# Kernel optimization log

Hardware: AMD Instinct MI355X
Metric: run time of the kernel (lower is better)

Reference implementation:

```python
import jax, jax.numpy as jnp
import numpy as np

N_HEAD, D_MODEL, D_HEAD, D_INNER = 16, 1024, 64, 4096
QLEN, BSZ = 2048, 2
LN_EPS = 1e-5
NEG_MIN = np.float32(np.finfo(np.float32).min)


def layer_norm(x, g, b, eps=LN_EPS):
    mu = jnp.mean(x, axis=-1, keepdims=True)
    var = jnp.var(x, axis=-1, keepdims=True)
    return (x - mu) * jax.lax.rsqrt(var + eps) * g + b


def rel_shift_uni(x):
    # x: [q, k, b, n] -> Transformer-XL relative shift
    q, k, b, n = x.shape
    zero_pad = jnp.zeros((q, 1, b, n), dtype=x.dtype)
    x_padded = jnp.concatenate([zero_pad, x], axis=1)        # [q, k+1, b, n]
    x_padded = x_padded.reshape(k + 1, q, b, n)
    return x_padded[1:].reshape(q, k, b, n)


def setup_inputs() -> dict:
    key = jax.random.key(0)
    ks = jax.random.split(key, 16)
    s = 0.02
    inp = {
        "dec_inp": jax.random.normal(ks[0], (QLEN, BSZ, D_MODEL), jnp.float32),
        "r": jax.random.normal(ks[1], (QLEN, D_MODEL), jnp.float32),
        "r_w_bias": jax.random.normal(ks[2], (N_HEAD, D_HEAD), jnp.float32) * s,
        "r_r_bias": jax.random.normal(ks[3], (N_HEAD, D_HEAD), jnp.float32) * s,
        "qkv_w": jax.random.normal(ks[4], (3 * N_HEAD * D_HEAD, D_MODEL), jnp.float32) * s,
        "r_net_w": jax.random.normal(ks[5], (N_HEAD * D_HEAD, D_MODEL), jnp.float32) * s,
        "o_w": jax.random.normal(ks[6], (D_MODEL, N_HEAD * D_HEAD), jnp.float32) * s,
        "ln_attn_g": jnp.ones((D_MODEL,), jnp.float32),
        "ln_attn_b": jnp.zeros((D_MODEL,), jnp.float32),
        "w1": jax.random.normal(ks[7], (D_INNER, D_MODEL), jnp.float32) * s,
        "b1": jnp.zeros((D_INNER,), jnp.float32),
        "w2": jax.random.normal(ks[8], (D_MODEL, D_INNER), jnp.float32) * s,
        "b2": jnp.zeros((D_MODEL,), jnp.float32),
        "ln_ff_g": jnp.ones((D_MODEL,), jnp.float32),
        "ln_ff_b": jnp.zeros((D_MODEL,), jnp.float32),
        # causal mask: mask position j > i; shape [q, k, 1]
        "attn_mask": jnp.triu(jnp.ones((QLEN, QLEN), bool), k=1)[:, :, None],
    }
    return inp


def reference(dec_inp, r, r_w_bias, r_r_bias, qkv_w, r_net_w, o_w,
              ln_attn_g, ln_attn_b, w1, b1, w2, b2, ln_ff_g, ln_ff_b,
              attn_mask):
    qlen, bsz = dec_inp.shape[0], dec_inp.shape[1]
    scale = 1.0 / (D_HEAD ** 0.5)

    # QKV projection (post-LN: no pre-norm)
    w_heads = jnp.einsum('ibm,hm->ibh', dec_inp, qkv_w)  # [q, b, 3*n*d]
    w_head_q, w_head_k, w_head_v = jnp.split(w_heads, 3, axis=-1)
    w_head_q = w_head_q.reshape(qlen, bsz, N_HEAD, D_HEAD)
    w_head_k = w_head_k.reshape(qlen, bsz, N_HEAD, D_HEAD)
    w_head_v = w_head_v.reshape(qlen, bsz, N_HEAD, D_HEAD)

    # content attention score (AC)
    rw_head_q = w_head_q + r_w_bias                      # [q, b, n, d]
    attn_score = jnp.einsum('ibnd,jbnd->ijbn', rw_head_q, w_head_k)

    # position attention score (BD) with relative shift
    rr_head_q = w_head_q + r_r_bias
    r_head_k = jnp.einsum('jm,hm->jh', r, r_net_w).reshape(qlen, N_HEAD, D_HEAD)
    BD = jnp.einsum('ibnd,jnd->ijbn', rr_head_q, r_head_k)
    BD = rel_shift_uni(BD)

    attn_score = (attn_score + BD) * scale
    attn_score = jnp.where(attn_mask[:, :, :, None], NEG_MIN, attn_score)

    attn_prob = jax.nn.softmax(attn_score, axis=1)       # softmax over key dim
    attn_vec = jnp.einsum('ijbn,jbnd->ibnd', attn_prob, w_head_v)
    attn_vec = attn_vec.reshape(qlen, bsz, N_HEAD * D_HEAD)
    attn_out = jnp.einsum('ibh,mh->ibm', attn_vec, o_w)

    # post-LN residual
    output = layer_norm(dec_inp + attn_out, ln_attn_g, ln_attn_b)

    # Positionwise FFN (post-LN)
    hidden = jax.nn.relu(jnp.einsum('ibm,fm->ibf', output, w1) + b1)
    core_out = jnp.einsum('ibf,mf->ibm', hidden, w2) + b2
    output = layer_norm(output + core_out, ln_ff_g, ln_ff_b)
    return output
```

## Files before the change

### kernel.cpp

```cpp
#include <hip/hip_runtime.h>
#include <stdint.h>

#define QL 2048
#define NHEAD 16
#define DHEAD 64
#define DMODEL 1024
#define DINNER 4096

typedef __attribute__((ext_vector_type(8))) short bf16x8;
typedef __attribute__((ext_vector_type(4))) float f32x4;

__device__ __forceinline__ ushort f2bf(float f) {
  uint32_t u = __float_as_uint(f);
  u = (u + 0x7fffu + ((u >> 16) & 1u)) >> 16;
  return (ushort)u;
}
__device__ __forceinline__ float bf2f(ushort u) {
  return __uint_as_float(((uint32_t)u) << 16);
}

__device__ __forceinline__ void gload_lds16(const void* g, void* l) {
  auto gp = reinterpret_cast<const uint32_t __attribute__((address_space(1)))*>(
      reinterpret_cast<uintptr_t>(g));
  auto lp = reinterpret_cast<uint32_t __attribute__((address_space(3)))*>(
      (uint32_t)reinterpret_cast<uintptr_t>(l));
  __builtin_amdgcn_global_load_lds(gp, lp, 16, 0, 0);
}

__global__ __launch_bounds__(256) void cvt_bf16_k(const float* __restrict__ in,
                                                  ushort* __restrict__ out, int n4) {
  int i = blockIdx.x * 256 + threadIdx.x;
  if (i < n4) {
    float4 v = ((const float4*)in)[i];
    ushort4 u;
    u.x = f2bf(v.x); u.y = f2bf(v.y); u.z = f2bf(v.z); u.w = f2bf(v.w);
    ((ushort4*)out)[i] = u;
  }
}

#define EPI_QKV 0
#define EPI_RK 1
#define EPI_F32 2
#define EPI_RELU_BF16 3
#define EPI_BIAS_F32 4

template <int EPI>
__global__ __launch_bounds__(256) void gemm_nt(
    const ushort* __restrict__ A, const ushort* __restrict__ B, int M, int N, int K,
    float* __restrict__ Cf, ushort* __restrict__ Cb, const float* __restrict__ bias,
    ushort* __restrict__ qw, ushort* __restrict__ qr, ushort* __restrict__ kbuf,
    ushort* __restrict__ vt, const float* __restrict__ rwb, const float* __restrict__ rrb) {
  __shared__ ushort As[2][128 * 32];
  __shared__ ushort Bs[2][128 * 32];
  const int t = threadIdx.x;
  const int lane = t & 63, wv = t >> 6;
  const int wr = wv >> 1, wc = wv & 1;
  const int m0 = blockIdx.y * 128, n0 = blockIdx.x * 128;
  const int rif = lane & 15;
  const int kb = (lane >> 4) * 16;

  f32x4 acc[4][4] = {};
  const char* Ab = (const char*)A;
  const char* Bb = (const char*)B;
  const int arow = t >> 2;
  const int acol = (t & 3) * 16;

  auto stage = [&](int b, int k0) {
    size_t abase = ((size_t)(m0 + arow) * K + k0) * 2 + acol;
    gload_lds16(Ab + abase, (char*)As[b] + t * 16);
    gload_lds16(Ab + abase + (size_t)64 * K * 2, (char*)As[b] + t * 16 + 4096);
    size_t bbase = ((size_t)(n0 + arow) * K + k0) * 2 + acol;
    gload_lds16(Bb + bbase, (char*)Bs[b] + t * 16);
    gload_lds16(Bb + bbase + (size_t)64 * K * 2, (char*)Bs[b] + t * 16 + 4096);
  };

  stage(0, 0);
  asm volatile("s_waitcnt vmcnt(0)" ::: "memory");
  __builtin_amdgcn_s_barrier();
  __builtin_amdgcn_sched_barrier(0);

  int cur = 0;
#pragma unroll 1
  for (int k0 = 0; k0 < K; k0 += 32) {
    if (k0 + 32 < K) stage(cur ^ 1, k0 + 32);
    bf16x8 af[4], bfr[4];
#pragma unroll
    for (int m = 0; m < 4; m++)
      af[m] = *(const bf16x8*)((const char*)As[cur] + (wr * 64 + m * 16 + rif) * 64 + kb);
#pragma unroll
    for (int n = 0; n < 4; n++)
      bfr[n] = *(const bf16x8*)((const char*)Bs[cur] + (wc * 64 + n * 16 + rif) * 64 + kb);
    __builtin_amdgcn_s_setprio(1);
#pragma unroll
    for (int m = 0; m < 4; m++)
#pragma unroll
      for (int n = 0; n < 4; n++)
        acc[m][n] = __builtin_amdgcn_mfma_f32_16x16x32_bf16(af[m], bfr[n], acc[m][n], 0, 0, 0);
    __builtin_amdgcn_s_setprio(0);
    asm volatile("s_waitcnt vmcnt(0)" ::: "memory");
    __builtin_amdgcn_s_barrier();
    __builtin_amdgcn_sched_barrier(0);
    cur ^= 1;
  }

  const int rbase = (lane >> 4) * 4;
#pragma unroll
  for (int m = 0; m < 4; m++) {
#pragma unroll
    for (int n = 0; n < 4; n++) {
#pragma unroll
      for (int reg = 0; reg < 4; reg++) {
        int gr = m0 + wr * 64 + m * 16 + rbase + reg;
        int gc = n0 + wc * 64 + n * 16 + (lane & 15);
        float v = acc[m][n][reg];
        if (EPI == EPI_F32) {
          Cf[(size_t)gr * N + gc] = v;
        } else if (EPI == EPI_BIAS_F32) {
          Cf[(size_t)gr * N + gc] = v + bias[gc];
        } else if (EPI == EPI_RELU_BF16) {
          Cb[(size_t)gr * N + gc] = f2bf(fmaxf(v + bias[gc], 0.f));
        } else if (EPI == EPI_RK) {
          int hn = gc >> 6, hd = gc & 63;
          Cb[((size_t)hn * QL + gr) * 64 + hd] = f2bf(v);
        } else {
          int which = gc >> 10, hh = gc & 1023;
          int hn = hh >> 6, hd = hh & 63;
          int qi = gr >> 1, qb = gr & 1;
          size_t off = ((size_t)(qb * NHEAD + hn) * QL + qi) * 64 + hd;
          if (which == 0) {
            qw[off] = f2bf(v + rwb[hh]);
            qr[off] = f2bf(v + rrb[hh]);
          } else if (which == 1) {
            kbuf[off] = f2bf(v);
          } else {
            vt[((size_t)(qb * NHEAD + hn) * 64 + hd) * QL + qi] = f2bf(v);
          }
        }
      }
    }
  }
}

template <int EPI>
__global__ __launch_bounds__(256) void gemm_nt64(
    const ushort* __restrict__ A, const ushort* __restrict__ B, int M, int N, int K,
    float* __restrict__ Cf, ushort* __restrict__ Cb, const float* __restrict__ bias) {
  __shared__ ushort As[2][128 * 32];
  __shared__ ushort Bs[2][64 * 32];
  const int t = threadIdx.x;
  const int lane = t & 63, wv = t >> 6;
  const int wr = wv >> 1, wc = wv & 1;
  const int m0 = blockIdx.y * 128, n0 = blockIdx.x * 64;
  const int rif = lane & 15;
  const int kb = (lane >> 4) * 16;

  f32x4 acc[4][2] = {};
  const char* Ab = (const char*)A;
  const char* Bb = (const char*)B;
  const int arow = t >> 2;
  const int acol = (t & 3) * 16;

  auto stage = [&](int b, int k0) {
    size_t abase = ((size_t)(m0 + arow) * K + k0) * 2 + acol;
    gload_lds16(Ab + abase, (char*)As[b] + t * 16);
    gload_lds16(Ab + abase + (size_t)64 * K * 2, (char*)As[b] + t * 16 + 4096);
    size_t bbase = ((size_t)(n0 + arow) * K + k0) * 2 + acol;
    gload_lds16(Bb + bbase, (char*)Bs[b] + t * 16);
  };

  stage(0, 0);
  asm volatile("s_waitcnt vmcnt(0)" ::: "memory");
  __builtin_amdgcn_s_barrier();
  __builtin_amdgcn_sched_barrier(0);

  int cur = 0;
#pragma unroll 1
  for (int k0 = 0; k0 < K; k0 += 32) {
    if (k0 + 32 < K) stage(cur ^ 1, k0 + 32);
    bf16x8 af[4], bfr[2];
#pragma unroll
    for (int m = 0; m < 4; m++)
      af[m] = *(const bf16x8*)((const char*)As[cur] + (wr * 64 + m * 16 + rif) * 64 + kb);
#pragma unroll
    for (int n = 0; n < 2; n++)
      bfr[n] = *(const bf16x8*)((const char*)Bs[cur] + (wc * 32 + n * 16 + rif) * 64 + kb);
    __builtin_amdgcn_s_setprio(1);
#pragma unroll
    for (int m = 0; m < 4; m++)
#pragma unroll
      for (int n = 0; n < 2; n++)
        acc[m][n] = __builtin_amdgcn_mfma_f32_16x16x32_bf16(af[m], bfr[n], acc[m][n], 0, 0, 0);
    __builtin_amdgcn_s_setprio(0);
    asm volatile("s_waitcnt vmcnt(0)" ::: "memory");
    __builtin_amdgcn_s_barrier();
    __builtin_amdgcn_sched_barrier(0);
    cur ^= 1;
  }

  const int rbase = (lane >> 4) * 4;
#pragma unroll
  for (int m = 0; m < 4; m++) {
#pragma unroll
    for (int n = 0; n < 2; n++) {
#pragma unroll
      for (int reg = 0; reg < 4; reg++) {
        int gr = m0 + wr * 64 + m * 16 + rbase + reg;
        int gc = n0 + wc * 32 + n * 16 + (lane & 15);
        float v = acc[m][n][reg];
        if (EPI == EPI_F32) {
          Cf[(size_t)gr * N + gc] = v;
        } else if (EPI == EPI_BIAS_F32) {
          Cf[(size_t)gr * N + gc] = v + bias[gc];
        } else {
          int hn = gc >> 6, hd = gc & 63;
          Cb[((size_t)hn * QL + gr) * 64 + hd] = f2bf(v);
        }
      }
    }
  }
}

__global__ __launch_bounds__(256) void flash_attn(
    const ushort* __restrict__ Qw, const ushort* __restrict__ Qr,
    const ushort* __restrict__ Kb, const ushort* __restrict__ Vt,
    const ushort* __restrict__ Rk, ushort* __restrict__ out) {
  __shared__ ushort K_lds[2][64 * 64];
  __shared__ ushort V_lds[2][64 * 64];
  __shared__ ushort R_lds[2][128 * 64];
  __shared__ ushort P_lds[4][16 * 64];

  const int t = threadIdx.x;
  const int lane = t & 63, wv = t >> 6;
  const int bn = blockIdx.y;
  const int qb = bn >> 4, hn = bn & 15;
  const int c4 = lane & 15, g4 = lane >> 4;

  const char* Qwb = (const char*)(Qw + (size_t)bn * QL * 64);
  const char* Qrb = (const char*)(Qr + (size_t)bn * QL * 64);
  const char* Kbb = (const char*)(Kb + (size_t)bn * QL * 64);
  const char* Vtb = (const char*)(Vt + (size_t)bn * 64 * QL);
  const char* Rkb = (const char*)(Rk + (size_t)hn * QL * 64);

  int addrs[4];
#pragma unroll
  for (int reg = 0; reg < 4; reg++) {
    int rr = g4 * 4 + reg;
    addrs[reg] = ((lane & 48) | ((c4 + 15 - rr) & 15)) << 2;
  }

  const float SCALE2 = 0.125f * 1.44269504088896340736f;

#pragma unroll 1
  for (int ph = 0; ph < 2; ph++) {
    const int itile = (ph == 0) ? (31 - (int)blockIdx.x) : (int)blockIdx.x;
    const int i0 = itile * 64;
    const int iw = i0 + wv * 16;
    const int niter = itile + 1;

    bf16x8 qwf[2], qrf[2];
#pragma unroll
    for (int kk = 0; kk < 2; kk++) {
      qwf[kk] = *(const bf16x8*)(Qwb + (size_t)(iw + c4) * 128 + kk * 64 + g4 * 16);
      qrf[kk] = *(const bf16x8*)(Qrb + (size_t)(iw + c4) * 128 + kk * 64 + g4 * 16);
    }

    f32x4 o_acc[4] = {};
    float m_run[4], l_run[4];
#pragma unroll
    for (int r = 0; r < 4; r++) { m_run[r] = -3.0e38f; l_run[r] = 0.f; }

    auto stage = [&](int b, int j0) {
      const int T0 = j0 - i0 + (QL - 64);
#pragma unroll
      for (int p = 0; p < 2; p++) {
        int o = t * 16 + p * 4096;
        int row = o >> 7, ch16 = ((((o & 127) >> 4) ^ (row & 7)) << 4);
        gload_lds16(Kbb + (size_t)(j0 + row) * 128 + ch16, (char*)K_lds[b] + o);
        gload_lds16(Vtb + (size_t)row * (QL * 2) + (size_t)j0 * 2 + ch16, (char*)V_lds[b] + o);
      }
#pragma unroll
      for (int p = 0; p < 4; p++) {
        int o = t * 16 + p * 4096;
        int r = o >> 7;
        int srow = T0 + r; srow = srow > QL - 1 ? QL - 1 : srow;
        int ch16 = ((((o & 127) >> 4) ^ (r & 7)) << 4);
        gload_lds16(Rkb + (size_t)srow * 128 + ch16, (char*)R_lds[b] + o);
      }
    };

    stage(0, 0);
    asm volatile("s_waitcnt vmcnt(0)" ::: "memory");
    __builtin_amdgcn_s_barrier();
    __builtin_amdgcn_sched_barrier(0);

    int cur = 0;
#pragma unroll 1
    for (int it = 0; it < niter; ++it) {
      const int j0 = it * 64;
      if (it + 1 < niter) stage(cur ^ 1, j0 + 64);

      f32x4 acc_s[4] = {};
      f32x4 acc_bd[5] = {};
      const int baseloc = 48 - wv * 16;
      __builtin_amdgcn_s_setprio(1);
#pragma unroll
      for (int kk = 0; kk < 2; kk++) {
        const int sw = (((kk * 4 + g4) ^ (c4 & 7)) << 4);
#pragma unroll
        for (int nf = 0; nf < 4; nf++) {
          bf16x8 bk = *(const bf16x8*)((const char*)K_lds[cur] + (nf * 16 + c4) * 128 + sw);
          acc_s[nf] = __builtin_amdgcn_mfma_f32_16x16x32_bf16(qwf[kk], bk, acc_s[nf], 0, 0, 0);
        }
#pragma unroll
        for (int tf = 0; tf < 5; tf++) {
          int oo = baseloc + tf * 16 + c4;
          bf16x8 br = *(const bf16x8*)((const char*)R_lds[cur] + oo * 128 + sw);
          acc_bd[tf] = __builtin_amdgcn_mfma_f32_16x16x32_bf16(qrf[kk], br, acc_bd[tf], 0, 0, 0);
        }
      }
      __builtin_amdgcn_s_setprio(0);

      uint32_t pk[4][4];
#pragma unroll
      for (int nf = 0; nf < 4; nf++)
#pragma unroll
        for (int reg = 0; reg < 4; reg++)
          asm("v_cvt_pk_bf16_f32 %0, %1, %2"
              : "=v"(pk[nf][reg])
              : "v"(acc_bd[nf][reg]), "v"(acc_bd[nf + 1][reg]));

      float sv[4][4];
      float rowmax[4] = {-3.0e38f, -3.0e38f, -3.0e38f, -3.0e38f};
#pragma unroll
      for (int nf = 0; nf < 4; nf++) {
#pragma unroll
        for (int reg = 0; reg < 4; reg++) {
          int rr = g4 * 4 + reg;
          int jg = j0 + nf * 16 + c4;
          int ig = iw + rr;
          uint32_t pulled = (uint32_t)__builtin_amdgcn_ds_bpermute(addrs[reg], (int)pk[nf][reg]);
          uint32_t bits = (c4 > rr) ? (pulled & 0xffff0000u) : (pulled << 16);
          float v = (acc_s[nf][reg] + __uint_as_float(bits)) * SCALE2;
          v = (jg <= ig) ? v : -3.0e38f;
          sv[nf][reg] = v;
          rowmax[reg] = fmaxf(rowmax[reg], v);
        }
      }
#pragma unroll
      for (int reg = 0; reg < 4; reg++) {
        float rm = rowmax[reg];
        rm = fmaxf(rm, __shfl_xor(rm, 1));
        rm = fmaxf(rm, __shfl_xor(rm, 2));
        rm = fmaxf(rm, __shfl_xor(rm, 4));
        rm = fmaxf(rm, __shfl_xor(rm, 8));
        float mnew = fmaxf(m_run[reg], rm);
        float alpha = __builtin_amdgcn_exp2f(m_run[reg] - mnew);
        float rsum = 0.f;
#pragma unroll
        for (int nf = 0; nf < 4; nf++) {
          float p = __builtin_amdgcn_exp2f(sv[nf][reg] - mnew);
          sv[nf][reg] = p;
          rsum += p;
        }
        rsum += __shfl_xor(rsum, 1);
        rsum += __shfl_xor(rsum, 2);
        rsum += __shfl_xor(rsum, 4);
        rsum += __shfl_xor(rsum, 8);
        l_run[reg] = l_run[reg] * alpha + rsum;
        m_run[reg] = mnew;
#pragma unroll
        for (int df = 0; df < 4; df++) o_acc[df][reg] *= alpha;
      }

      {
        char* pb = (char*)P_lds[wv];
#pragma unroll
        for (int nf = 0; nf < 4; nf++)
#pragma unroll
          for (int reg = 0; reg < 4; reg++) {
            int row = g4 * 4 + reg, col = nf * 16 + c4;
            int byt = row * 128 + ((((col >> 3) ^ (row & 7))) << 4) + (col & 7) * 2;
            *(ushort*)(pb + byt) = f2bf(sv[nf][reg]);
          }
      }
      __builtin_amdgcn_s_setprio(1);
#pragma unroll
      for (int kk = 0; kk < 2; kk++) {
        const char* pb = (const char*)P_lds[wv];
        bf16x8 pa = *(const bf16x8*)(pb + c4 * 128 + (((kk * 4 + g4) ^ (c4 & 7)) << 4));
        const int sw = (((kk * 4 + g4) ^ (c4 & 7)) << 4);
#pragma unroll
        for (int df = 0; df < 4; df++) {
          bf16x8 bv = *(const bf16x8*)((const char*)V_lds[cur] + (df * 16 + c4) * 128 + sw);
          o_acc[df] = __builtin_amdgcn_mfma_f32_16x16x32_bf16(pa, bv, o_acc[df], 0, 0, 0);
        }
      }
      __builtin_amdgcn_s_setprio(0);

      asm volatile("s_waitcnt vmcnt(0)" ::: "memory");
      __builtin_amdgcn_s_barrier();
      __builtin_amdgcn_sched_barrier(0);
      cur ^= 1;
    }

#pragma unroll
    for (int reg = 0; reg < 4; reg++) {
      float inv = 1.0f / l_run[reg];
      int ig = iw + g4 * 4 + reg;
      size_t grow = (size_t)(ig * 2 + qb) * 1024 + hn * 64;
#pragma unroll
      for (int df = 0; df < 4; df++)
        out[grow + df * 16 + c4] = f2bf(o_acc[df][reg] * inv);
    }
  }
}

template <bool WB>
__global__ __launch_bounds__(256) void ln_res(
    const float* __restrict__ xa, const float* __restrict__ xb,
    const float* __restrict__ g, const float* __restrict__ bt,
    float* __restrict__ of, ushort* __restrict__ ob) {
  __shared__ float red[8];
  const int row = blockIdx.x;
  const int t = threadIdx.x;
  const int lane = t & 63, wv = t >> 6;
  const float4 a = *(const float4*)(xa + (size_t)row * 1024 + t * 4);
  const float4 c = *(const float4*)(xb + (size_t)row * 1024 + t * 4);
  float x[4] = {a.x + c.x, a.y + c.y, a.z + c.z, a.w + c.w};
  float s = x[0] + x[1] + x[2] + x[3];
  for (int m = 1; m < 64; m <<= 1) s += __shfl_xor(s, m);
  if (lane == 0) red[wv] = s;
  __syncthreads();
  float mu = (red[0] + red[1] + red[2] + red[3]) * (1.f / 1024.f);
  float d[4];
  float ss = 0.f;
#pragma unroll
  for (int i = 0; i < 4; i++) { d[i] = x[i] - mu; ss += d[i] * d[i]; }
  for (int m = 1; m < 64; m <<= 1) ss += __shfl_xor(ss, m);
  if (lane == 0) red[4 + wv] = ss;
  __syncthreads();
  float var = (red[4] + red[5] + red[6] + red[7]) * (1.f / 1024.f);
  float rs = rsqrtf(var + 1e-5f);
  float4 gv = *(const float4*)(g + t * 4);
  float4 bv = *(const float4*)(bt + t * 4);
  float y[4] = {d[0] * rs * gv.x + bv.x, d[1] * rs * gv.y + bv.y,
                d[2] * rs * gv.z + bv.z, d[3] * rs * gv.w + bv.w};
  float4 yo = make_float4(y[0], y[1], y[2], y[3]);
  *(float4*)(of + (size_t)row * 1024 + t * 4) = yo;
  if (WB) {
    ushort4 u;
    u.x = f2bf(y[0]); u.y = f2bf(y[1]); u.z = f2bf(y[2]); u.w = f2bf(y[3]);
    *(ushort4*)(ob + (size_t)row * 1024 + t * 4) = u;
  }
}

extern "C" void kernel_launch(void* const* d_in, const int* in_sizes, int n_in,
                              void* d_out, int out_size, void* d_ws, size_t ws_size,
                              hipStream_t stream) {
  const float* dec_inp = (const float*)d_in[0];
  const float* r_in = (const float*)d_in[1];
  const float* rwb = (const float*)d_in[2];
  const float* rrb = (const float*)d_in[3];
  const float* qkv_w = (const float*)d_in[4];
  const float* rnet_w = (const float*)d_in[5];
  const float* o_w = (const float*)d_in[6];
  const float* ln_attn_g = (const float*)d_in[7];
  const float* ln_attn_b = (const float*)d_in[8];
  const float* w1 = (const float*)d_in[9];
  const float* b1 = (const float*)d_in[10];
  const float* w2 = (const float*)d_in[11];
  const float* b2 = (const float*)d_in[12];
  const float* ln_ff_g = (const float*)d_in[13];
  const float* ln_ff_b = (const float*)d_in[14];
  float* out = (float*)d_out;

  char* ws = (char*)d_ws;
  size_t off = 0;
  auto alloc = [&](size_t bytes) {
    char* p = ws + off;
    off += (bytes + 255) & ~(size_t)255;
    return p;
  };
  const int ROWS = QL * 2;
  ushort* qkvw_b = (ushort*)alloc((size_t)3072 * 1024 * 2);
  ushort* rnetw_b = (ushort*)alloc((size_t)1024 * 1024 * 2);
  ushort* ow_b = (ushort*)alloc((size_t)1024 * 1024 * 2);
  ushort* w1_b = (ushort*)alloc((size_t)4096 * 1024 * 2);
  ushort* w2_b = (ushort*)alloc((size_t)1024 * 4096 * 2);
  ushort* x_b = (ushort*)alloc((size_t)ROWS * 1024 * 2);
  ushort* r_b = (ushort*)alloc((size_t)QL * 1024 * 2);
  ushort* Qw = (ushort*)alloc((size_t)32 * QL * 64 * 2);
  ushort* Qr = (ushort*)alloc((size_t)32 * QL * 64 * 2);
  ushort* Kb = (ushort*)alloc((size_t)32 * QL * 64 * 2);
  ushort* Vt = (ushort*)alloc((size_t)32 * 64 * QL * 2);
  ushort* rk = (ushort*)alloc((size_t)16 * QL * 64 * 2);
  ushort* avec = (ushort*)alloc((size_t)ROWS * 1024 * 2);
  float* attn_out = (float*)alloc((size_t)ROWS * 1024 * 4);
  float* x1f = (float*)alloc((size_t)ROWS * 1024 * 4);
  ushort* x1b = (ushort*)alloc((size_t)ROWS * 1024 * 2);
  ushort* hidden = (ushort*)alloc((size_t)ROWS * 4096 * 2);
  float* core = (float*)alloc((size_t)ROWS * 1024 * 4);

  auto cvt = [&](const float* src, ushort* dst, int n) {
    int n4 = n / 4;
    cvt_bf16_k<<<n4 / 256, 256, 0, stream>>>(src, dst, n4);
  };
  cvt(qkv_w, qkvw_b, 3072 * 1024);
  cvt(rnet_w, rnetw_b, 1024 * 1024);
  cvt(o_w, ow_b, 1024 * 1024);
  cvt(w1, w1_b, 4096 * 1024);
  cvt(w2, w2_b, 1024 * 4096);
  cvt(dec_inp, x_b, ROWS * 1024);
  cvt(r_in, r_b, QL * 1024);

  gemm_nt<EPI_QKV><<<dim3(3072 / 128, ROWS / 128), 256, 0, stream>>>(
      x_b, qkvw_b, ROWS, 3072, 1024, nullptr, nullptr, nullptr, Qw, Qr, Kb, Vt, rwb, rrb);
  gemm_nt64<EPI_RK><<<dim3(1024 / 64, QL / 128), 256, 0, stream>>>(
      r_b, rnetw_b, QL, 1024, 1024, nullptr, rk, nullptr);
  flash_attn<<<dim3(16, 32), 256, 0, stream>>>(Qw, Qr, Kb, Vt, rk, avec);
  gemm_nt64<EPI_F32><<<dim3(1024 / 64, ROWS / 128), 256, 0, stream>>>(
      avec, ow_b, ROWS, 1024, 1024, attn_out, nullptr, nullptr);
  ln_res<true><<<ROWS, 256, 0, stream>>>(dec_inp, attn_out, ln_attn_g, ln_attn_b, x1f, x1b);
  gemm_nt<EPI_RELU_BF16><<<dim3(4096 / 128, ROWS / 128), 256, 0, stream>>>(
      x1b, w1_b, ROWS, 4096, 1024, nullptr, hidden, b1, nullptr, nullptr, nullptr, nullptr,
      nullptr, nullptr);
  gemm_nt64<EPI_BIAS_F32><<<dim3(1024 / 64, ROWS / 128), 256, 0, stream>>>(
      hidden, w2_b, ROWS, 1024, 4096, core, nullptr, b2);
  ln_res<false><<<ROWS, 256, 0, stream>>>(x1f, core, ln_ff_g, ln_ff_b, out, nullptr);
}
```

Measured before the change: 358.4 us.

## Split-K output GEMMs, smaller-tile r-projection, and single fused conversion kernel

Measured after the change: 350.1 us. 2.3% less time.

```diff
diff --git a/kernel.cpp b/kernel.cpp
--- a/kernel.cpp
+++ b/kernel.cpp
@@ -14,9 +14,6 @@
   uint32_t u = __float_as_uint(f);
   u = (u + 0x7fffu + ((u >> 16) & 1u)) >> 16;
   return (ushort)u;
-}
-__device__ __forceinline__ float bf2f(ushort u) {
-  return __uint_as_float(((uint32_t)u) << 16);
 }
 
 __device__ __forceinline__ void gload_lds16(const void* g, void* l) {
@@ -27,22 +24,29 @@
   __builtin_amdgcn_global_load_lds(gp, lp, 16, 0, 0);
 }
 
-__global__ __launch_bounds__(256) void cvt_bf16_k(const float* __restrict__ in,
-                                                  ushort* __restrict__ out, int n4) {
-  int i = blockIdx.x * 256 + threadIdx.x;
-  if (i < n4) {
-    float4 v = ((const float4*)in)[i];
+struct CvtArgs {
+  const float* src[7];
+  ushort* dst[7];
+  int end[7];
+};
+
+__global__ __launch_bounds__(256) void cvt_all_k(CvtArgs a, int total4) {
+  for (int i = blockIdx.x * 256 + threadIdx.x; i < total4; i += gridDim.x * 256) {
+    int seg = 0;
+#pragma unroll
+    for (int s = 0; s < 6; s++)
+      if (i >= a.end[s]) seg = s + 1;
+    int base = seg ? a.end[seg - 1] : 0;
+    int j = i - base;
+    float4 v = ((const float4*)a.src[seg])[j];
     ushort4 u;
     u.x = f2bf(v.x); u.y = f2bf(v.y); u.z = f2bf(v.z); u.w = f2bf(v.w);
-    ((ushort4*)out)[i] = u;
+    ((ushort4*)a.dst[seg])[j] = u;
   }
 }
 
 #define EPI_QKV 0
-#define EPI_RK 1
-#define EPI_F32 2
 #define EPI_RELU_BF16 3
-#define EPI_BIAS_F32 4
 
 template <int EPI>
 __global__ __launch_bounds__(256) void gemm_nt(
@@ -113,15 +117,8 @@
         int gr = m0 + wr * 64 + m * 16 + rbase + reg;
         int gc = n0 + wc * 64 + n * 16 + (lane & 15);
         float v = acc[m][n][reg];
-        if (EPI == EPI_F32) {
-          Cf[(size_t)gr * N + gc] = v;
-        } else if (EPI == EPI_BIAS_F32) {
-          Cf[(size_t)gr * N + gc] = v + bias[gc];
-        } else if (EPI == EPI_RELU_BF16) {
+        if (EPI == EPI_RELU_BF16) {
           Cb[(size_t)gr * N + gc] = f2bf(fmaxf(v + bias[gc], 0.f));
-        } else if (EPI == EPI_RK) {
-          int hn = gc >> 6, hd = gc & 63;
-          Cb[((size_t)hn * QL + gr) * 64 + hd] = f2bf(v);
         } else {
           int which = gc >> 10, hh = gc & 1023;
           int hn = hh >> 6, hd = hh & 63;
@@ -141,16 +138,20 @@
   }
 }
 
-template <int EPI>
-__global__ __launch_bounds__(256) void gemm_nt64(
-    const ushort* __restrict__ A, const ushort* __restrict__ B, int M, int N, int K,
-    float* __restrict__ Cf, ushort* __restrict__ Cb, const float* __restrict__ bias) {
+template <int WITH_BIAS>
+__global__ __launch_bounds__(256) void gemm_nt64sk(
+    const ushort* __restrict__ A, const ushort* __restrict__ B, int M, int N, int Kfull,
+    int Klen, float* __restrict__ Cf0, float* __restrict__ Cf1,
+    const float* __restrict__ bias) {
   __shared__ ushort As[2][128 * 32];
   __shared__ ushort Bs[2][64 * 32];
   const int t = threadIdx.x;
   const int lane = t & 63, wv = t >> 6;
   const int wr = wv >> 1, wc = wv & 1;
   const int m0 = blockIdx.y * 128, n0 = blockIdx.x * 64;
+  const int z = blockIdx.z;
+  const int koff = z * Klen;
+  float* Cf = z ? Cf1 : Cf0;
   const int rif = lane & 15;
   const int kb = (lane >> 4) * 16;
 
@@ -161,10 +162,10 @@
   const int acol = (t & 3) * 16;
 
   auto stage = [&](int b, int k0) {
-    size_t abase = ((size_t)(m0 + arow) * K + k0) * 2 + acol;
+    size_t abase = ((size_t)(m0 + arow) * Kfull + koff + k0) * 2 + acol;
     gload_lds16(Ab + abase, (char*)As[b] + t * 16);
-    gload_lds16(Ab + abase + (size_t)64 * K * 2, (char*)As[b] + t * 16 + 4096);
-    size_t bbase = ((size_t)(n0 + arow) * K + k0) * 2 + acol;
+    gload_lds16(Ab + abase + (size_t)64 * Kfull * 2, (char*)As[b] + t * 16 + 4096);
+    size_t bbase = ((size_t)(n0 + arow) * Kfull + koff + k0) * 2 + acol;
     gload_lds16(Bb + bbase, (char*)Bs[b] + t * 16);
   };
 
@@ -175,8 +176,8 @@
 
   int cur = 0;
 #pragma unroll 1
-  for (int k0 = 0; k0 < K; k0 += 32) {
-    if (k0 + 32 < K) stage(cur ^ 1, k0 + 32);
+  for (int k0 = 0; k0 < Klen; k0 += 32) {
+    if (k0 + 32 < Klen) stage(cur ^ 1, k0 + 32);
     bf16x8 af[4], bfr[2];
 #pragma unroll
     for (int m = 0; m < 4; m++)
@@ -207,14 +208,78 @@
         int gr = m0 + wr * 64 + m * 16 + rbase + reg;
         int gc = n0 + wc * 32 + n * 16 + (lane & 15);
         float v = acc[m][n][reg];
-        if (EPI == EPI_F32) {
-          Cf[(size_t)gr * N + gc] = v;
-        } else if (EPI == EPI_BIAS_F32) {
-          Cf[(size_t)gr * N + gc] = v + bias[gc];
-        } else {
-          int hn = gc >> 6, hd = gc & 63;
-          Cb[((size_t)hn * QL + gr) * 64 + hd] = f2bf(v);
-        }
+        if (WITH_BIAS && z == 0) v += bias[gc];
+        Cf[(size_t)gr * N + gc] = v;
+      }
+    }
+  }
+}
+
+__global__ __launch_bounds__(256) void gemm_rk64(
+    const ushort* __restrict__ A, const ushort* __restrict__ B, int M, int N, int K,
+    ushort* __restrict__ Cb) {
+  __shared__ ushort As[2][64 * 32];
+  __shared__ ushort Bs[2][64 * 32];
+  const int t = threadIdx.x;
+  const int lane = t & 63, wv = t >> 6;
+  const int wr = wv >> 1, wc = wv & 1;
+  const int m0 = blockIdx.y * 64, n0 = blockIdx.x * 64;
+  const int rif = lane & 15;
+  const int kb = (lane >> 4) * 16;
+
+  f32x4 acc[2][2] = {};
+  const char* Ab = (const char*)A;
+  const char* Bb = (const char*)B;
+  const int arow = t >> 2;
+  const int acol = (t & 3) * 16;
+
+  auto stage = [&](int b, int k0) {
+    size_t abase = ((size_t)(m0 + arow) * K + k0) * 2 + acol;
+    gload_lds16(Ab + abase, (char*)As[b] + t * 16);
+    size_t bbase = ((size_t)(n0 + arow) * K + k0) * 2 + acol;
+    gload_lds16(Bb + bbase, (char*)Bs[b] + t * 16);
+  };
+
+  stage(0, 0);
+  asm volatile("s_waitcnt vmcnt(0)" ::: "memory");
+  __builtin_amdgcn_s_barrier();
+  __builtin_amdgcn_sched_barrier(0);
+
+  int cur = 0;
+#pragma unroll 1
+  for (int k0 = 0; k0 < K; k0 += 32) {
+    if (k0 + 32 < K) stage(cur ^ 1, k0 + 32);
+    bf16x8 af[2], bfr[2];
+#pragma unroll
+    for (int m = 0; m < 2; m++)
+      af[m] = *(const bf16x8*)((const char*)As[cur] + (wr * 32 + m * 16 + rif) * 64 + kb);
+#pragma unroll
+    for (int n = 0; n < 2; n++)
+      bfr[n] = *(const bf16x8*)((const char*)Bs[cur] + (wc * 32 + n * 16 + rif) * 64 + kb);
+    __builtin_amdgcn_s_setprio(1);
+#pragma unroll
+    for (int m = 0; m < 2; m++)
+#pragma unroll
+      for (int n = 0; n < 2; n++)
+        acc[m][n] = __builtin_amdgcn_mfma_f32_16x16x32_bf16(af[m], bfr[n], acc[m][n], 0, 0, 0);
+    __builtin_amdgcn_s_setprio(0);
+    asm volatile("s_waitcnt vmcnt(0)" ::: "memory");
+    __builtin_amdgcn_s_barrier();
+    __builtin_amdgcn_sched_barrier(0);
+    cur ^= 1;
+  }
+
+  const int rbase = (lane >> 4) * 4;
+#pragma unroll
+  for (int m = 0; m < 2; m++) {
+#pragma unroll
+    for (int n = 0; n < 2; n++) {
+#pragma unroll
+      for (int reg = 0; reg < 4; reg++) {
+        int gr = m0 + wr * 32 + m * 16 + rbase + reg;
+        int gc = n0 + wc * 32 + n * 16 + (lane & 15);
+        int hn = gc >> 6, hd = gc & 63;
+        Cb[((size_t)hn * QL + gr) * 64 + hd] = f2bf(acc[m][n][reg]);
       }
     }
   }
@@ -416,17 +481,18 @@
 }
 
 template <bool WB>
-__global__ __launch_bounds__(256) void ln_res(
-    const float* __restrict__ xa, const float* __restrict__ xb,
-    const float* __restrict__ g, const float* __restrict__ bt,
-    float* __restrict__ of, ushort* __restrict__ ob) {
+__global__ __launch_bounds__(256) void ln_res3(
+    const float* __restrict__ xa, const float* __restrict__ xb0,
+    const float* __restrict__ xb1, const float* __restrict__ g,
+    const float* __restrict__ bt, float* __restrict__ of, ushort* __restrict__ ob) {
   __shared__ float red[8];
   const int row = blockIdx.x;
   const int t = threadIdx.x;
   const int lane = t & 63, wv = t >> 6;
   const float4 a = *(const float4*)(xa + (size_t)row * 1024 + t * 4);
-  const float4 c = *(const float4*)(xb + (size_t)row * 1024 + t * 4);
-  float x[4] = {a.x + c.x, a.y + c.y, a.z + c.z, a.w + c.w};
+  const float4 c0 = *(const float4*)(xb0 + (size_t)row * 1024 + t * 4);
+  const float4 c1 = *(const float4*)(xb1 + (size_t)row * 1024 + t * 4);
+  float x[4] = {a.x + c0.x + c1.x, a.y + c0.y + c1.y, a.z + c0.z + c1.z, a.w + c0.w + c1.w};
   float s = x[0] + x[1] + x[2] + x[3];
   for (int m = 1; m < 64; m <<= 1) s += __shfl_xor(s, m);
   if (lane == 0) red[wv] = s;
@@ -495,36 +561,39 @@
   ushort* Vt = (ushort*)alloc((size_t)32 * 64 * QL * 2);
   ushort* rk = (ushort*)alloc((size_t)16 * QL * 64 * 2);
   ushort* avec = (ushort*)alloc((size_t)ROWS * 1024 * 2);
-  float* attn_out = (float*)alloc((size_t)ROWS * 1024 * 4);
+  float* p0 = (float*)alloc((size_t)ROWS * 1024 * 4);
+  float* p1 = (float*)alloc((size_t)ROWS * 1024 * 4);
   float* x1f = (float*)alloc((size_t)ROWS * 1024 * 4);
   ushort* x1b = (ushort*)alloc((size_t)ROWS * 1024 * 2);
   ushort* hidden = (ushort*)alloc((size_t)ROWS * 4096 * 2);
-  float* core = (float*)alloc((size_t)ROWS * 1024 * 4);
-
-  auto cvt = [&](const float* src, ushort* dst, int n) {
-    int n4 = n / 4;
-    cvt_bf16_k<<<n4 / 256, 256, 0, stream>>>(src, dst, n4);
-  };
-  cvt(qkv_w, qkvw_b, 3072 * 1024);
-  cvt(rnet_w, rnetw_b, 1024 * 1024);
-  cvt(o_w, ow_b, 1024 * 1024);
-  cvt(w1, w1_b, 4096 * 1024);
-  cvt(w2, w2_b, 1024 * 4096);
-  cvt(dec_inp, x_b, ROWS * 1024);
-  cvt(r_in, r_b, QL * 1024);
+  float* q0 = (float*)alloc((size_t)ROWS * 1024 * 4);
+  float* q1 = (float*)alloc((size_t)ROWS * 1024 * 4);
+
+  CvtArgs ca;
+  int n4[7] = {3072 * 1024 / 4, 1024 * 1024 / 4, 1024 * 1024 / 4, 4096 * 1024 / 4,
+               1024 * 4096 / 4, ROWS * 1024 / 4, QL * 1024 / 4};
+  const float* srcs[7] = {qkv_w, rnet_w, o_w, w1, w2, dec_inp, r_in};
+  ushort* dsts[7] = {qkvw_b, rnetw_b, ow_b, w1_b, w2_b, x_b, r_b};
+  int cum = 0;
+  for (int i = 0; i < 7; i++) {
+    ca.src[i] = srcs[i];
+    ca.dst[i] = dsts[i];
+    cum += n4[i];
+    ca.end[i] = cum;
+  }
+  cvt_all_k<<<2048, 256, 0, stream>>>(ca, cum);
 
   gemm_nt<EPI_QKV><<<dim3(3072 / 128, ROWS / 128), 256, 0, stream>>>(
       x_b, qkvw_b, ROWS, 3072, 1024, nullptr, nullptr, nullptr, Qw, Qr, Kb, Vt, rwb, rrb);
-  gemm_nt64<EPI_RK><<<dim3(1024 / 64, QL / 128), 256, 0, stream>>>(
-      r_b, rnetw_b, QL, 1024, 1024, nullptr, rk, nullptr);
+  gemm_rk64<<<dim3(1024 / 64, QL / 64), 256, 0, stream>>>(r_b, rnetw_b, QL, 1024, 1024, rk);
   flash_attn<<<dim3(16, 32), 256, 0, stream>>>(Qw, Qr, Kb, Vt, rk, avec);
-  gemm_nt64<EPI_F32><<<dim3(1024 / 64, ROWS / 128), 256, 0, stream>>>(
-      avec, ow_b, ROWS, 1024, 1024, attn_out, nullptr, nullptr);
-  ln_res<true><<<ROWS, 256, 0, stream>>>(dec_inp, attn_out, ln_attn_g, ln_attn_b, x1f, x1b);
+  gemm_nt64sk<0><<<dim3(1024 / 64, ROWS / 128, 2), 256, 0, stream>>>(
+      avec, ow_b, ROWS, 1024, 1024, 512, p0, p1, nullptr);
+  ln_res3<true><<<ROWS, 256, 0, stream>>>(dec_inp, p0, p1, ln_attn_g, ln_attn_b, x1f, x1b);
   gemm_nt<EPI_RELU_BF16><<<dim3(4096 / 128, ROWS / 128), 256, 0, stream>>>(
       x1b, w1_b, ROWS, 4096, 1024, nullptr, hidden, b1, nullptr, nullptr, nullptr, nullptr,
       nullptr, nullptr);
-  gemm_nt64<EPI_BIAS_F32><<<dim3(1024 / 64, ROWS / 128), 256, 0, stream>>>(
-      hidden, w2_b, ROWS, 1024, 4096, core, nullptr, b2);
-  ln_res<false><<<ROWS, 256, 0, stream>>>(x1f, core, ln_ff_g, ln_ff_b, out, nullptr);
-}
+  gemm_nt64sk<1><<<dim3(1024 / 64, ROWS / 128, 2), 256, 0, stream>>>(
+      hidden, w2_b, ROWS, 1024, 4096, 2048, q0, q1, b2);
+  ln_res3<false><<<ROWS, 256, 0, stream>>>(x1f, q0, q1, ln_ff_g, ln_ff_b, out, nullptr);
+}
```
